# Kernel tuning notes

Measured on AMD Instinct MI355X. Metric: run time of the kernel, lower is better.

## Reference

```python
import jax, jax.numpy as jnp
import numpy as np

NUM_HEADS = 8
EPS = 1e-3

N_TOKENS = 32768
DIM = 256
N_WIN = 128
WIN = N_TOKENS // N_WIN  # 256 tokens per window


def setup_inputs() -> dict:
    key = jax.random.key(0)
    ks = jax.random.split(key, 4)
    x = jax.random.normal(ks[0], (N_TOKENS, DIM), dtype=jnp.float32)
    # torch nn.Linear weights are [out_features, in_features]
    w_qkv = jax.random.normal(ks[1], (3 * DIM, DIM), dtype=jnp.float32) * (DIM ** -0.5)
    w_proj = jax.random.normal(ks[2], (DIM, DIM), dtype=jnp.float32) * (DIM ** -0.5)
    b_proj = jnp.zeros((DIM,), dtype=jnp.float32)
    batch_win_inds = (jnp.arange(N_TOKENS) // WIN).astype(jnp.int64)
    offsets = (jnp.arange(N_WIN) * WIN).astype(jnp.int64)
    counts = jnp.full((N_WIN,), WIN, dtype=jnp.int64)
    return {"x": x, "w_qkv": w_qkv, "w_proj": w_proj, "b_proj": b_proj,
            "offsets": offsets, "counts": counts, "batch_win_inds": batch_win_inds}


def reference(x, w_qkv, w_proj, b_proj, offsets, counts, batch_win_inds):
    N, C = x.shape
    H = NUM_HEADS
    hd = C // H
    W = counts.shape[0]  # number of windows (static)

    qkv = x @ w_qkv.T                      # [N, 3C]
    q, k, v = jnp.split(qkv, 3, axis=-1)   # each [N, C]
    q = jax.nn.relu(q.reshape(N, H, hd))   # [N, H, hd]
    k = jax.nn.relu(k.reshape(N, H, hd))
    v = v.reshape(N, H, hd)

    seg = batch_win_inds.astype(jnp.int32)
    # per-window KV state: kv[w] = sum_{i in w} k_i^T v_i   -> [W, H, hd, hd]
    kv = jax.ops.segment_sum(jnp.einsum('nhc,nhd->nhcd', k, v), seg, num_segments=W)
    # per-window key sum for normalizer                      -> [W, H, hd]
    s = jax.ops.segment_sum(k, seg, num_segments=W)

    y = jnp.einsum('nhc,nhcd->nhd', q, kv[seg])              # [N, H, hd]
    z = jnp.sum(s[seg] * q, axis=-1, keepdims=True)          # [N, H, 1]
    y = y / (z + EPS)

    y = y.reshape(N, C) @ w_proj.T + b_proj                  # [N, C]
    return y
```

## Files before the change

### kernel.cpp

```cpp
#include <hip/hip_runtime.h>

typedef __bf16 bf16_t;
typedef bf16_t bf16x8 __attribute__((ext_vector_type(8)));
typedef bf16_t bf16x4 __attribute__((ext_vector_type(4)));
typedef float f32x4 __attribute__((ext_vector_type(4)));

#define M_TOK 32768
#define NWIN 128
#define WIN  256

typedef __attribute__((address_space(3))) void* as3p;
typedef const __attribute__((address_space(1))) void* as1p;

__device__ __forceinline__ void gll16(const void* g, void* l) {
    __builtin_amdgcn_global_load_lds((as1p)g, (as3p)l, 16, 0, 0);
}

__device__ __forceinline__ bf16x8 cvt8(f32x4 a, f32x4 b) {
    bf16x8 o;
    o[0] = (bf16_t)a[0]; o[1] = (bf16_t)a[1]; o[2] = (bf16_t)a[2]; o[3] = (bf16_t)a[3];
    o[4] = (bf16_t)b[0]; o[5] = (bf16_t)b[1]; o[6] = (bf16_t)b[2]; o[7] = (bf16_t)b[3];
    return o;
}

__global__ __launch_bounds__(256) void wconv(
    const float* __restrict__ wq, const float* __restrict__ wp,
    bf16_t* __restrict__ wqb, bf16_t* __restrict__ wpb)
{
    int i4 = (blockIdx.x * 256 + threadIdx.x) * 4;
    const float* s; bf16_t* dst; int idx;
    if (i4 < 196608) { s = wq; dst = wqb; idx = i4; }
    else             { s = wp; dst = wpb; idx = i4 - 196608; }
    f32x4 v = *(const f32x4*)(s + idx);
    bf16x4 o;
    o[0] = (bf16_t)v[0]; o[1] = (bf16_t)v[1]; o[2] = (bf16_t)v[2]; o[3] = (bf16_t)v[3];
    *(bf16x4*)(dst + idx) = o;
}

__global__ __launch_bounds__(256) void gemm1_qkv(
    const float* __restrict__ X,
    const bf16_t* __restrict__ Wb,
    bf16_t* __restrict__ QKV)
{
    __shared__ __align__(16) bf16_t As[2][128][32];
    __shared__ __align__(16) bf16_t Bs[2][128][32];

    const int tid = threadIdx.x;
    const int lane = tid & 63;
    const int wv = tid >> 6;
    const int wm = wv >> 1, wn = wv & 1;
    const int id = blockIdx.x;
    const int sg = id / 48, wsub = id % 48;
    const int m0 = (sg * 8 + (wsub & 7)) * 128;
    const int n0 = (wsub >> 3) * 128;
    const int r = lane & 15, q = lane >> 4;
    const int lrow = lane >> 2;
    const int lcol = lane & 3;
    const int sgr = (lcol ^ ((lane >> 3) & 3)) * 8;
    const int ax8 = (q ^ ((r >> 1) & 3)) * 8;

    f32x4 acc[4][4] = {};

    auto loadA = [&](int kc, f32x4 (&ar)[2][2]) {
#pragma unroll
        for (int g = 0; g < 2; ++g) {
            const float* src = X + (size_t)(m0 + wv * 32 + g * 16 + lrow) * 256 + kc + sgr;
            ar[g][0] = *(const f32x4*)src;
            ar[g][1] = *(const f32x4*)(src + 4);
        }
    };
    auto stageB = [&](int kc, int buf) {
#pragma unroll
        for (int g = 0; g < 2; ++g)
            gll16(Wb + (size_t)(n0 + wv * 32 + g * 16 + lrow) * 256 + kc + sgr,
                  &Bs[buf][wv * 32 + g * 16][0]);
    };
    auto writeA = [&](f32x4 (&ar)[2][2], int buf) {
#pragma unroll
        for (int g = 0; g < 2; ++g)
            *(bf16x8*)&As[buf][wv * 32 + g * 16 + lrow][lcol * 8] = cvt8(ar[g][0], ar[g][1]);
    };
    auto compute = [&](int buf) {
        bf16x8 a[4], b[4];
#pragma unroll
        for (int i = 0; i < 4; ++i)
            a[i] = *(const bf16x8*)&As[buf][wm * 64 + i * 16 + r][ax8];
#pragma unroll
        for (int j = 0; j < 4; ++j)
            b[j] = *(const bf16x8*)&Bs[buf][wn * 64 + j * 16 + r][ax8];
#pragma unroll
        for (int i = 0; i < 4; ++i)
#pragma unroll
            for (int j = 0; j < 4; ++j)
                acc[i][j] = __builtin_amdgcn_mfma_f32_16x16x32_bf16(b[j], a[i], acc[i][j], 0, 0, 0);
    };

    {
        f32x4 ar[2][2];
        loadA(0, ar);
        stageB(0, 0);
        writeA(ar, 0);
    }
    __syncthreads();

#pragma unroll
    for (int t = 0; t < 7; ++t) {
        const int cur = t & 1, nxt = cur ^ 1;
        f32x4 ar[2][2];
        loadA((t + 1) * 32, ar);
        stageB((t + 1) * 32, nxt);
        compute(cur);
        writeA(ar, nxt);
        __syncthreads();
    }
    compute(1);

#pragma unroll
    for (int i = 0; i < 4; ++i) {
        const int rowg = m0 + wm * 64 + i * 16 + r;
#pragma unroll
        for (int j = 0; j < 4; ++j) {
            const int nb = n0 + wn * 64 + j * 16 + q * 4;
            const int nblk = nb >> 5, d = nb & 31;
            bf16x4 o;
#pragma unroll
            for (int reg = 0; reg < 4; ++reg) {
                float v = acc[i][j][reg];
                if (nblk < 16) v = fmaxf(v, 0.0f);
                o[reg] = (bf16_t)v;
            }
            *(bf16x4*)&QKV[((size_t)nblk * M_TOK + rowg) * 32 + d] = o;
        }
    }
}

__global__ __launch_bounds__(256) void gemm2_proj(
    const bf16_t* __restrict__ Y,
    const bf16_t* __restrict__ Wb,
    const float* __restrict__ bias,
    float* __restrict__ Out)
{
    __shared__ __align__(16) bf16_t As[2][128][32];
    __shared__ __align__(16) bf16_t Bs[2][64][32];

    const int tid = threadIdx.x;
    const int lane = tid & 63;
    const int wv = tid >> 6;
    const int wm = wv >> 1, wn = wv & 1;
    const int id = blockIdx.x;
    const int sg = id / 32, wsub = id % 32;
    const int m0 = (sg * 8 + (wsub & 7)) * 128;
    const int n0 = (wsub >> 3) * 64;
    const int r = lane & 15, q = lane >> 4;
    const int lrow = lane >> 2;
    const int sgr = ((lane & 3) ^ ((lane >> 3) & 3)) * 8;
    const int ax8 = (q ^ ((r >> 1) & 3)) * 8;

    f32x4 acc[4][2] = {};

    auto stage = [&](int kc, int buf) {
#pragma unroll
        for (int g = 0; g < 2; ++g)
            gll16(Y + (size_t)(m0 + wv * 32 + g * 16 + lrow) * 256 + kc + sgr,
                  &As[buf][wv * 32 + g * 16][0]);
        gll16(Wb + (size_t)(n0 + wv * 16 + lrow) * 256 + kc + sgr,
              &Bs[buf][wv * 16][0]);
    };
    auto compute = [&](int buf) {
        bf16x8 a[4], b[2];
#pragma unroll
        for (int i = 0; i < 4; ++i)
            a[i] = *(const bf16x8*)&As[buf][wm * 64 + i * 16 + r][ax8];
#pragma unroll
        for (int j = 0; j < 2; ++j)
            b[j] = *(const bf16x8*)&Bs[buf][wn * 32 + j * 16 + r][ax8];
#pragma unroll
        for (int i = 0; i < 4; ++i)
#pragma unroll
            for (int j = 0; j < 2; ++j)
                acc[i][j] = __builtin_amdgcn_mfma_f32_16x16x32_bf16(b[j], a[i], acc[i][j], 0, 0, 0);
    };

    stage(0, 0);
    __syncthreads();
#pragma unroll
    for (int t = 0; t < 7; ++t) {
        const int cur = t & 1, nxt = cur ^ 1;
        stage((t + 1) * 32, nxt);
        compute(cur);
        __syncthreads();
    }
    compute(1);

#pragma unroll
    for (int i = 0; i < 4; ++i) {
        const int rowg = m0 + wm * 64 + i * 16 + r;
#pragma unroll
        for (int j = 0; j < 2; ++j) {
            const int nb = n0 + wn * 32 + j * 16 + q * 4;
            f32x4 bi = *(const f32x4*)(bias + nb);
            f32x4 o;
#pragma unroll
            for (int reg = 0; reg < 4; ++reg) o[reg] = acc[i][j][reg] + bi[reg];
            *(f32x4*)&Out[(size_t)rowg * 256 + nb] = o;
        }
    }
}

__global__ __launch_bounds__(256) void kvy_kernel(
    const bf16_t* __restrict__ QKV,
    const int* __restrict__ offsets,
    const int* __restrict__ counts,
    bf16_t* __restrict__ Y)
{
    const int w = blockIdx.x;
    const int h = blockIdx.y;
    const int is64 = (counts[1] == 0) ? 1 : 0;
    const int off = offsets[w << is64];
    const int tid = threadIdx.x;
    const int lane = tid & 63;
    const int wv = tid >> 6;

    __shared__ __align__(16) bf16_t KT[32 * 264];
    __shared__ __align__(16) bf16_t VT[32 * 264];
    __shared__ __align__(16) bf16_t KVT[32 * 40];
    __shared__ float sbuf[32];
    __shared__ float spart[32 * 8];
    __shared__ float zinv[WIN];

    {
        const int t = tid;
        const bf16_t* kp = QKV + ((size_t)(8 + h) * M_TOK + off + t) * 32;
        const bf16_t* vp = QKV + ((size_t)(16 + h) * M_TOK + off + t) * 32;
        bf16_t ka[32], va[32];
#pragma unroll
        for (int u = 0; u < 4; ++u) {
            bf16x8 kk = *(const bf16x8*)(kp + u * 8);
            bf16x8 vvv = *(const bf16x8*)(vp + u * 8);
#pragma unroll
            for (int j = 0; j < 8; ++j) { ka[u * 8 + j] = kk[j]; va[u * 8 + j] = vvv[j]; }
        }
#pragma unroll
        for (int c = 0; c < 32; ++c) {
            KT[c * 264 + t] = ka[c];
            VT[c * 264 + t] = va[c];
        }
    }
    __syncthreads();

    {
        const int c = tid >> 3;
        const int tc = (tid & 7) * 32;
        float ps = 0.f;
#pragma unroll
        for (int u = 0; u < 4; ++u) {
            bf16x8 kk = *(const bf16x8*)(&KT[c * 264 + tc + u * 8]);
#pragma unroll
            for (int j = 0; j < 8; ++j) ps += (float)kk[j];
        }
        spart[c * 8 + (tid & 7)] = ps;
    }
    {
        const int i = wv >> 1, j = wv & 1;
        const int r = lane & 15, q = lane >> 4;
        f32x4 acc = {};
#pragma unroll
        for (int ch = 0; ch < 8; ++ch) {
            bf16x8 af = *(const bf16x8*)(&KT[(i * 16 + r) * 264 + ch * 32 + q * 8]);
            bf16x8 bf_ = *(const bf16x8*)(&VT[(j * 16 + r) * 264 + ch * 32 + q * 8]);
            acc = __builtin_amdgcn_mfma_f32_16x16x32_bf16(af, bf_, acc, 0, 0, 0);
        }
        bf16x4 kv4;
#pragma unroll
        for (int reg = 0; reg < 4; ++reg) kv4[reg] = (bf16_t)acc[reg];
        *(bf16x4*)(&KVT[(j * 16 + r) * 40 + i * 16 + q * 4]) = kv4;
    }
    __syncthreads();
    if (tid < 32) {
        float s = 0.f;
#pragma unroll
        for (int u = 0; u < 8; ++u) s += spart[tid * 8 + u];
        sbuf[tid] = s;
    }
    __syncthreads();

    {
        const int t = tid;
        const bf16_t* qp = QKV + ((size_t)h * M_TOK + off + t) * 32;
        float z = 0.f;
#pragma unroll
        for (int u = 0; u < 4; ++u) {
            bf16x8 qq = *(const bf16x8*)(qp + u * 8);
#pragma unroll
            for (int j = 0; j < 8; ++j) z += (float)qq[j] * sbuf[u * 8 + j];
        }
        zinv[t] = 1.0f / (z + 1e-3f);
    }
    __syncthreads();

    {
        const int r = lane & 15, q = lane >> 4;
        bf16x8 b0 = *(const bf16x8*)(&KVT[(r) * 40 + q * 8]);
        bf16x8 b1 = *(const bf16x8*)(&KVT[(16 + r) * 40 + q * 8]);
#pragma unroll
        for (int u = 0; u < 4; ++u) {
            const int mi = wv * 4 + u;
            const bf16_t* ap = QKV + ((size_t)h * M_TOK + off + mi * 16 + r) * 32 + q * 8;
            bf16x8 af = *(const bf16x8*)ap;
            f32x4 acc0 = {}, acc1 = {};
            acc0 = __builtin_amdgcn_mfma_f32_16x16x32_bf16(b0, af, acc0, 0, 0, 0);
            acc1 = __builtin_amdgcn_mfma_f32_16x16x32_bf16(b1, af, acc1, 0, 0, 0);
            const int tkn = mi * 16 + r;
            const float zi = zinv[tkn];
            bf16_t* yp = Y + (size_t)(off + tkn) * 256 + h * 32;
            bf16x4 o0, o1;
#pragma unroll
            for (int reg = 0; reg < 4; ++reg) {
                o0[reg] = (bf16_t)(acc0[reg] * zi);
                o1[reg] = (bf16_t)(acc1[reg] * zi);
            }
            *(bf16x4*)(yp + q * 4) = o0;
            *(bf16x4*)(yp + 16 + q * 4) = o1;
        }
    }
}

extern "C" void kernel_launch(void* const* d_in, const int* in_sizes, int n_in,
                              void* d_out, int out_size, void* d_ws, size_t ws_size,
                              hipStream_t stream) {
    const float* x      = (const float*)d_in[0];
    const float* w_qkv  = (const float*)d_in[1];
    const float* w_proj = (const float*)d_in[2];
    const float* b_proj = (const float*)d_in[3];
    const int*   offs   = (const int*)d_in[4];
    const int*   cnts   = (const int*)d_in[5];

    char* ws = (char*)d_ws;
    bf16_t* QKV = (bf16_t*)ws;
    bf16_t* Y   = (bf16_t*)(ws + 50331648);
    bf16_t* Wqb = (bf16_t*)(ws + 67108864);
    bf16_t* Wpb = (bf16_t*)(ws + 67502080);
    float*  out = (float*)d_out;

    wconv<<<256, 256, 0, stream>>>(w_qkv, w_proj, Wqb, Wpb);

    gemm1_qkv<<<1536, 256, 0, stream>>>(x, Wqb, QKV);

    kvy_kernel<<<dim3(NWIN, 8), 256, 0, stream>>>(QKV, offs, cnts, Y);

    gemm2_proj<<<1024, 256, 0, stream>>>(Y, Wpb, b_proj, out);
}
```

Before: 149.2 us.

## Triple-buffer GEMM staging with async LDS loads and explicit vmcnt waits

Both projection GEMMs move from double-buffered to triple-buffered LDS staging. Three K-chunks are issued up front and each step waits with s_waitcnt vmcnt instead of a full __syncthreads drain. In the QKV GEMM, the fp32 X tile is now copied straight into LDS with global_load_lds and converted to bf16 at fragment-read time, replacing the register load, convert and store path. This deepens load/compute overlap but doubles the A-tile LDS footprint, which may lower occupancy, and adds convert work inside the inner loop.

```diff
diff --git a/kernel.cpp b/kernel.cpp
--- a/kernel.cpp
+++ b/kernel.cpp
@@ -22,6 +22,9 @@
     o[4] = (bf16_t)b[0]; o[5] = (bf16_t)b[1]; o[6] = (bf16_t)b[2]; o[7] = (bf16_t)b[3];
     return o;
 }
+
+#define VMW_(n) asm volatile("s_waitcnt vmcnt(" #n ")" ::: "memory")
+#define VMW(n) VMW_(n)
 
 __global__ __launch_bounds__(256) void wconv(
     const float* __restrict__ wq, const float* __restrict__ wp,
@@ -42,8 +45,8 @@
     const bf16_t* __restrict__ Wb,
     bf16_t* __restrict__ QKV)
 {
-    __shared__ __align__(16) bf16_t As[2][128][32];
-    __shared__ __align__(16) bf16_t Bs[2][128][32];
+    __shared__ __align__(16) float  As[3][128][32];
+    __shared__ __align__(16) bf16_t Bs[3][128][32];
 
     const int tid = threadIdx.x;
     const int lane = tid & 63;
@@ -54,40 +57,40 @@
     const int m0 = (sg * 8 + (wsub & 7)) * 128;
     const int n0 = (wsub >> 3) * 128;
     const int r = lane & 15, q = lane >> 4;
-    const int lrow = lane >> 2;
-    const int lcol = lane & 3;
-    const int sgr = (lcol ^ ((lane >> 3) & 3)) * 8;
-    const int ax8 = (q ^ ((r >> 1) & 3)) * 8;
+    const int arow = lane >> 3;
+    const int ag = (lane & 7) ^ arow;
+    const int brow = lane >> 2;
+    const int bg = (lane & 3) ^ (brow & 3);
 
     f32x4 acc[4][4] = {};
 
-    auto loadA = [&](int kc, f32x4 (&ar)[2][2]) {
-#pragma unroll
-        for (int g = 0; g < 2; ++g) {
-            const float* src = X + (size_t)(m0 + wv * 32 + g * 16 + lrow) * 256 + kc + sgr;
-            ar[g][0] = *(const f32x4*)src;
-            ar[g][1] = *(const f32x4*)(src + 4);
-        }
-    };
-    auto stageB = [&](int kc, int buf) {
-#pragma unroll
-        for (int g = 0; g < 2; ++g)
-            gll16(Wb + (size_t)(n0 + wv * 32 + g * 16 + lrow) * 256 + kc + sgr,
-                  &Bs[buf][wv * 32 + g * 16][0]);
-    };
-    auto writeA = [&](f32x4 (&ar)[2][2], int buf) {
-#pragma unroll
-        for (int g = 0; g < 2; ++g)
-            *(bf16x8*)&As[buf][wv * 32 + g * 16 + lrow][lcol * 8] = cvt8(ar[g][0], ar[g][1]);
+    auto stage = [&](int t, int buf) {
+        const int kc = t * 32;
+#pragma unroll
+        for (int u = 0; u < 4; ++u) {
+            const int rb = wv * 32 + u * 8;
+            gll16(X + (size_t)(m0 + rb + arow) * 256 + kc + ag * 4, &As[buf][rb][0]);
+        }
+#pragma unroll
+        for (int u = 0; u < 2; ++u) {
+            const int rb = wv * 32 + u * 16;
+            gll16(Wb + (size_t)(n0 + rb + brow) * 256 + kc + bg * 8, &Bs[buf][rb][0]);
+        }
     };
     auto compute = [&](int buf) {
         bf16x8 a[4], b[4];
 #pragma unroll
-        for (int i = 0; i < 4; ++i)
-            a[i] = *(const bf16x8*)&As[buf][wm * 64 + i * 16 + r][ax8];
+        for (int i = 0; i < 4; ++i) {
+            const int row = wm * 64 + i * 16 + r;
+            const int g0 = (2 * q) ^ (r & 7);
+            const int g1 = (2 * q + 1) ^ (r & 7);
+            f32x4 lo = *(const f32x4*)&As[buf][row][g0 * 4];
+            f32x4 hi = *(const f32x4*)&As[buf][row][g1 * 4];
+            a[i] = cvt8(lo, hi);
+        }
 #pragma unroll
         for (int j = 0; j < 4; ++j)
-            b[j] = *(const bf16x8*)&Bs[buf][wn * 64 + j * 16 + r][ax8];
+            b[j] = *(const bf16x8*)&Bs[buf][wn * 64 + j * 16 + r][(q ^ (r & 3)) * 8];
 #pragma unroll
         for (int i = 0; i < 4; ++i)
 #pragma unroll
@@ -95,25 +98,21 @@
                 acc[i][j] = __builtin_amdgcn_mfma_f32_16x16x32_bf16(b[j], a[i], acc[i][j], 0, 0, 0);
     };
 
-    {
-        f32x4 ar[2][2];
-        loadA(0, ar);
-        stageB(0, 0);
-        writeA(ar, 0);
-    }
-    __syncthreads();
-
-#pragma unroll
-    for (int t = 0; t < 7; ++t) {
-        const int cur = t & 1, nxt = cur ^ 1;
-        f32x4 ar[2][2];
-        loadA((t + 1) * 32, ar);
-        stageB((t + 1) * 32, nxt);
-        compute(cur);
-        writeA(ar, nxt);
-        __syncthreads();
-    }
-    compute(1);
+    stage(0, 0); stage(1, 1); stage(2, 2);
+
+#define G1_STEP(t, NW) do { \
+        VMW(NW); \
+        __builtin_amdgcn_s_barrier(); \
+        __builtin_amdgcn_sched_barrier(0); \
+        compute((t) % 3); \
+        __builtin_amdgcn_sched_barrier(0); \
+        __builtin_amdgcn_s_barrier(); \
+        if ((t) + 3 < 8) stage((t) + 3, (t) % 3); \
+    } while (0)
+
+    G1_STEP(0, 12); G1_STEP(1, 12); G1_STEP(2, 12); G1_STEP(3, 12);
+    G1_STEP(4, 12); G1_STEP(5, 12); G1_STEP(6, 6);  G1_STEP(7, 0);
+#undef G1_STEP
 
 #pragma unroll
     for (int i = 0; i < 4; ++i) {
@@ -140,8 +139,8 @@
     const float* __restrict__ bias,
     float* __restrict__ Out)
 {
-    __shared__ __align__(16) bf16_t As[2][128][32];
-    __shared__ __align__(16) bf16_t Bs[2][64][32];
+    __shared__ __align__(16) bf16_t As[3][128][32];
+    __shared__ __align__(16) bf16_t Bs[3][64][32];
 
     const int tid = threadIdx.x;
     const int lane = tid & 63;
@@ -152,28 +151,28 @@
     const int m0 = (sg * 8 + (wsub & 7)) * 128;
     const int n0 = (wsub >> 3) * 64;
     const int r = lane & 15, q = lane >> 4;
-    const int lrow = lane >> 2;
-    const int sgr = ((lane & 3) ^ ((lane >> 3) & 3)) * 8;
-    const int ax8 = (q ^ ((r >> 1) & 3)) * 8;
+    const int brow = lane >> 2;
+    const int bg = (lane & 3) ^ (brow & 3);
 
     f32x4 acc[4][2] = {};
 
-    auto stage = [&](int kc, int buf) {
-#pragma unroll
-        for (int g = 0; g < 2; ++g)
-            gll16(Y + (size_t)(m0 + wv * 32 + g * 16 + lrow) * 256 + kc + sgr,
-                  &As[buf][wv * 32 + g * 16][0]);
-        gll16(Wb + (size_t)(n0 + wv * 16 + lrow) * 256 + kc + sgr,
-              &Bs[buf][wv * 16][0]);
+    auto stage = [&](int t, int buf) {
+        const int kc = t * 32;
+#pragma unroll
+        for (int u = 0; u < 2; ++u) {
+            const int rb = wv * 32 + u * 16;
+            gll16(Y + (size_t)(m0 + rb + brow) * 256 + kc + bg * 8, &As[buf][rb][0]);
+        }
+        gll16(Wb + (size_t)(n0 + wv * 16 + brow) * 256 + kc + bg * 8, &Bs[buf][wv * 16][0]);
     };
     auto compute = [&](int buf) {
         bf16x8 a[4], b[2];
 #pragma unroll
         for (int i = 0; i < 4; ++i)
-            a[i] = *(const bf16x8*)&As[buf][wm * 64 + i * 16 + r][ax8];
+            a[i] = *(const bf16x8*)&As[buf][wm * 64 + i * 16 + r][(q ^ (r & 3)) * 8];
 #pragma unroll
         for (int j = 0; j < 2; ++j)
-            b[j] = *(const bf16x8*)&Bs[buf][wn * 32 + j * 16 + r][ax8];
+            b[j] = *(const bf16x8*)&Bs[buf][wn * 32 + j * 16 + r][(q ^ (r & 3)) * 8];
 #pragma unroll
         for (int i = 0; i < 4; ++i)
 #pragma unroll
@@ -181,16 +180,21 @@
                 acc[i][j] = __builtin_amdgcn_mfma_f32_16x16x32_bf16(b[j], a[i], acc[i][j], 0, 0, 0);
     };
 
-    stage(0, 0);
-    __syncthreads();
-#pragma unroll
-    for (int t = 0; t < 7; ++t) {
-        const int cur = t & 1, nxt = cur ^ 1;
-        stage((t + 1) * 32, nxt);
-        compute(cur);
-        __syncthreads();
-    }
-    compute(1);
+    stage(0, 0); stage(1, 1); stage(2, 2);
+
+#define G2_STEP(t, NW) do { \
+        VMW(NW); \
+        __builtin_amdgcn_s_barrier(); \
+        __builtin_amdgcn_sched_barrier(0); \
+        compute((t) % 3); \
+        __builtin_amdgcn_sched_barrier(0); \
+        __builtin_amdgcn_s_barrier(); \
+        if ((t) + 3 < 8) stage((t) + 3, (t) % 3); \
+    } while (0)
+
+    G2_STEP(0, 6); G2_STEP(1, 6); G2_STEP(2, 6); G2_STEP(3, 6);
+    G2_STEP(4, 6); G2_STEP(5, 6); G2_STEP(6, 3); G2_STEP(7, 0);
+#undef G2_STEP
 
 #pragma unroll
     for (int i = 0; i < 4; ++i) {
```

Measured after the change: 145.4 us. -2.5%, faster.
